# Kernel tuning notes

Hardware: AMD Instinct MI355X
Metric: run time of the kernel (lower is better)

The kernel has to match this reference:

```python
import jax, jax.numpy as jnp
import numpy as np

N = 65536      # nodes in batched graph
E = 2097152    # edges (avg degree 32)
V = 1000       # chord vocabulary size
F_IN = 128     # chord feature dim
H = 256        # hidden_dim
OUT = 128      # out_dim
G = 256        # number of graphs in batch


def _gcn_layer(x, W, b, row, col, norm, n):
    # x: [n, f_in] -> [n, f_out]; PyG GCNConv: linear then normalized aggregation + bias
    x = x @ W
    msg = x[row] * norm[:, None]            # gather at source, scale by sym-norm
    return jax.ops.segment_sum(msg, col, num_segments=n) + b


def setup_inputs() -> dict:
    key = jax.random.key(0)
    ks = jax.random.split(key, 9)
    chord_feats = jax.random.normal(ks[0], (V, F_IN), jnp.float32)
    W1 = jax.random.normal(ks[1], (F_IN, H), jnp.float32) * 0.05
    b1 = jnp.zeros((H,), jnp.float32)
    W2 = jax.random.normal(ks[2], (H, OUT), jnp.float32) * 0.05
    b2 = jnp.zeros((OUT,), jnp.float32)
    edge_attr = jax.random.uniform(ks[3], (E,), jnp.float32)          # positive edge weights
    node_indices = jax.random.randint(ks[4], (N,), 0, V, jnp.int64)
    edge_index = jax.random.randint(ks[5], (2, E), 0, N, jnp.int64)
    batch_index = jnp.sort(jax.random.randint(ks[6], (N,), 0, G, jnp.int64))
    return {"chord_feats": chord_feats, "W1": W1, "b1": b1, "W2": W2, "b2": b2,
            "edge_attr": edge_attr, "node_indices": node_indices,
            "edge_index": edge_index, "batch_index": batch_index}


def reference(chord_feats, W1, b1, W2, b2, edge_attr, node_indices, edge_index, batch_index):
    loops = jnp.arange(N, dtype=edge_index.dtype)
    row = jnp.concatenate([edge_index[0], loops])   # source
    col = jnp.concatenate([edge_index[1], loops])   # target
    ew = jnp.concatenate([edge_attr, jnp.ones((N,), edge_attr.dtype)])  # self-loop weight 1
    # symmetric GCN normalization: D^-1/2 A D^-1/2
    deg = jax.ops.segment_sum(ew, col, num_segments=N)
    dis = jnp.where(deg > 0, jax.lax.rsqrt(jnp.maximum(deg, 1e-30)), 0.0)
    norm = dis[row] * ew * dis[col]

    x = chord_feats[node_indices]                   # [N, F_IN]
    x = jax.nn.relu(_gcn_layer(x, W1, b1, row, col, norm, N))
    x = jax.nn.relu(_gcn_layer(x, W2, b2, row, col, norm, N))

    # global_mean_pool over batch_index
    sums = jax.ops.segment_sum(x, batch_index, num_segments=G)
    counts = jax.ops.segment_sum(jnp.ones((N,), x.dtype), batch_index, num_segments=G)
    return sums / jnp.maximum(counts, 1.0)[:, None]
```

## Files before the change

kernel.cpp:

```cpp
#include <hip/hip_runtime.h>
#include <hip/hip_fp16.h>
#include <math.h>

constexpr int N_NODES = 65536;
constexpr int N_EDGES = 2097152;
constexpr int F_IN    = 128;
constexpr int H_DIM   = 256;
constexpr int O_DIM   = 128;
constexpr int N_GRAPH = 256;
constexpr int V_SIZE  = 1000;

constexpr int EPB  = 8192;
constexpr int NBLK = N_EDGES / EPB;
constexpr float FXP = 16777216.0f;

typedef _Float16 half8 __attribute__((ext_vector_type(8)));
typedef float floatx4 __attribute__((ext_vector_type(4)));


__global__ void k_init(float* __restrict__ pool, const int* __restrict__ batch,
                       float* __restrict__ cntf, const float* __restrict__ cf,
                       const float* __restrict__ W1, __half* __restrict__ cfW1,
                       const float* __restrict__ W2, _Float16* __restrict__ W2T) {
    __shared__ float xs[8 * F_IN];
    int i = blockIdx.x * blockDim.x + threadIdx.x;
    if (i < N_GRAPH * O_DIM) pool[i] = 0.0f;
    if (blockIdx.x == 0) {
        int g = threadIdx.x;
        int lo = 0, hi = N_NODES;
        while (lo < hi) { int m = (lo + hi) >> 1; if (batch[m] < g) lo = m + 1; else hi = m; }
        int start = lo;
        lo = 0; hi = N_NODES;
        while (lo < hi) { int m = (lo + hi) >> 1; if (batch[m] <= g) lo = m + 1; else hi = m; }
        cntf[g] = (float)(lo - start);
    }
    if (blockIdx.x < V_SIZE / 8) {
        int rb = blockIdx.x * 8;
        int t  = threadIdx.x;
        #pragma unroll
        for (int p = 0; p < 4; ++p) {
            int idx = p * 256 + t;
            int r = idx >> 7, k = idx & 127;
            xs[idx] = cf[(size_t)(rb + r) * F_IN + k];
        }
        __syncthreads();
        float acc[8] = {};
        for (int k = 0; k < F_IN; ++k) {
            float w = W1[k * H_DIM + t];
            #pragma unroll
            for (int j = 0; j < 8; ++j) acc[j] += xs[j * F_IN + k] * w;
        }
        #pragma unroll
        for (int j = 0; j < 8; ++j)
            cfW1[(size_t)(rb + j) * H_DIM + t] = __float2half(acc[j]);
    }
    if (blockIdx.x >= 128) {
        int idx = (blockIdx.x - 128) * 256 + threadIdx.x;
        int nn = idx >> 8, kk = idx & 255;
        W2T[idx] = (_Float16)W2[kk * O_DIM + nn];
    }
}


__global__ void k_hist(const int* __restrict__ col, int* __restrict__ hist) {
    __shared__ int h[256];
    int t = threadIdx.x;
    h[t] = 0;
    __syncthreads();
    int base = blockIdx.x * EPB;
    #pragma unroll
    for (int i = 0; i < EPB / 256; ++i)
        atomicAdd(&h[col[base + i * 256 + t] >> 8], 1);
    __syncthreads();
    hist[t * NBLK + blockIdx.x] = h[t];
}


__global__ void k_scan1(const int* __restrict__ in, int* __restrict__ out,
                        int* __restrict__ bsum) {
    __shared__ int s[256];
    int tid = threadIdx.x;
    int i = blockIdx.x * 256 + tid;
    int v = in[i];
    s[tid] = v;
    __syncthreads();
    for (int d = 1; d < 256; d <<= 1) {
        int t = (tid >= d) ? s[tid - d] : 0;
        __syncthreads();
        s[tid] += t;
        __syncthreads();
    }
    out[i] = s[tid] - v;
    if (tid == 255) bsum[blockIdx.x] = s[255];
}

__global__ void k_scan2(int* __restrict__ bsum) {
    __shared__ int s[256];
    int tid = threadIdx.x;
    int v = bsum[tid];
    s[tid] = v;
    __syncthreads();
    for (int d = 1; d < 256; d <<= 1) {
        int t = (tid >= d) ? s[tid - d] : 0;
        __syncthreads();
        s[tid] += t;
        __syncthreads();
    }
    bsum[tid] = s[tid] - v;
}


__global__ void k_part(const int* __restrict__ row, const int* __restrict__ col,
                       const float* __restrict__ ew, const int* __restrict__ nidx,
                       const int* __restrict__ hoffs, const int* __restrict__ bsum,
                       int2* __restrict__ part) {
    __shared__ int cur[256];
    int t = threadIdx.x;
    cur[t] = hoffs[t * NBLK + blockIdx.x] + bsum[t];
    __syncthreads();
    int base = blockIdx.x * EPB;
    for (int i = 0; i < EPB / 256; ++i) {
        int e = base + i * 256 + t;
        int r = row[e], c = col[e];
        unsigned hw = (unsigned)__half_as_ushort(__float2half(ew[e]));
        int vb = nidx[r];
        int slot = atomicAdd(&cur[c >> 8], 1);
        int2 rec;
        rec.x = (r << 16) | ((c & 255) << 8) | (vb >> 2);
        rec.y = (int)(((unsigned)(vb & 3) << 16) | hw);
        part[slot] = rec;
    }
}


__global__ void k_build1(const int* __restrict__ hoffs, const int* __restrict__ bsum,
                         const int2* __restrict__ part, float* __restrict__ dis,
                         int* __restrict__ offs) {
    __shared__ unsigned long long dc[256];
    __shared__ int sc[256];
    int t = threadIdx.x;
    int bucket = blockIdx.x;
    dc[t] = 0ULL;
    __syncthreads();
    int start = hoffs[bucket * NBLK] + bsum[bucket];
    int end   = (bucket == 255) ? N_EDGES : (hoffs[(bucket + 1) * NBLK] + bsum[bucket + 1]);
    for (int j = start + t; j < end; j += 256) {
        int2 rec = part[j];
        int dst = (rec.x >> 8) & 255;
        float w = __half2float(__ushort_as_half((unsigned short)(rec.y & 0xFFFF)));
        atomicAdd(&dc[dst], (1ULL << 40) |
                  (unsigned long long)(unsigned)(w * FXP + 0.5f));
    }
    __syncthreads();
    unsigned long long v = dc[t];
    float deg = 1.0f + (float)(v & 0xFFFFFFFFFFULL) * (1.0f / FXP);
    dis[bucket * 256 + t] = 1.0f / sqrtf(deg);
    int cnt = (int)(v >> 40);
    sc[t] = cnt;
    __syncthreads();
    for (int d = 1; d < 256; d <<= 1) {
        int x = (t >= d) ? sc[t - d] : 0;
        __syncthreads();
        sc[t] += x;
        __syncthreads();
    }
    offs[bucket * 256 + t] = start + sc[t] - cnt;
    if (bucket == 255 && t == 255) offs[N_NODES] = N_EDGES;
}


__global__ void k_build2(const int* __restrict__ hoffs, const int* __restrict__ bsum,
                         const int2* __restrict__ part, const float* __restrict__ dis,
                         const int* __restrict__ offs, int2* __restrict__ csr) {
    __shared__ int cur[256];
    int t = threadIdx.x;
    int bucket = blockIdx.x;
    cur[t] = offs[bucket * 256 + t];
    __syncthreads();
    int start = hoffs[bucket * NBLK] + bsum[bucket];
    int end   = (bucket == 255) ? N_EDGES : (hoffs[(bucket + 1) * NBLK] + bsum[bucket + 1]);
    for (int j = start + t; j < end; j += 256) {
        int2 rec = part[j];
        int dst = (rec.x >> 8) & 255;
        unsigned src = ((unsigned)rec.x) >> 16;
        int vb = ((rec.x & 255) << 2) | ((rec.y >> 16) & 3);
        float w = __half2float(__ushort_as_half((unsigned short)(rec.y & 0xFFFF)));
        float nm = dis[src] * w;
        int slot = atomicAdd(&cur[dst], 1);
        int2 e;
        e.x = (int)((src << 10) | (unsigned)vb);
        e.y = __float_as_int(nm);
        csr[slot] = e;
    }
}

__device__ __forceinline__ void acc8(float* e, int4 v, float n) {
    float2 f0 = __half22float2(*(__half2*)&v.x);
    float2 f1 = __half22float2(*(__half2*)&v.y);
    float2 f2 = __half22float2(*(__half2*)&v.z);
    float2 f3 = __half22float2(*(__half2*)&v.w);
    e[0] += f0.x * n; e[1] += f0.y * n;
    e[2] += f1.x * n; e[3] += f1.y * n;
    e[4] += f2.x * n; e[5] += f2.y * n;
    e[6] += f3.x * n; e[7] += f3.y * n;
}


__global__ void __launch_bounds__(256) k_agg1g2(
        const int4* __restrict__ cfW1, const int* __restrict__ nidx,
        const float* __restrict__ dis, const int* __restrict__ offs,
        const int2* __restrict__ csr, const float4* __restrict__ b1f4,
        const _Float16* __restrict__ W2T, __half* __restrict__ xw2h) {
    __shared__ _Float16 h1s[16 * 264];
    int wave = threadIdx.x >> 6;
    int lane = threadIdx.x & 63;
    int g    = lane >> 5;
    int sl   = lane & 31;
    int rowbase = blockIdx.x * 16;

    float4 bb0 = b1f4[2 * sl];
    float4 bb1 = b1f4[2 * sl + 1];

    for (int j = 0; j < 4; ++j) {
        int c = rowbase + wave * 4 + j;
        float d = dis[c];
        int4 sp = cfW1[(size_t)nidx[c] * 32 + sl];
        float esum[8] = {0.f, 0.f, 0.f, 0.f, 0.f, 0.f, 0.f, 0.f};
        int a0 = offs[c], a1 = offs[c + 1];
        int s = a0;
        if (s < a1 && (s & 1)) {
            int sb = __builtin_amdgcn_readfirstlane(s);
            int2 e0 = csr[sb];
            int4 v0 = cfW1[(size_t)(e0.x & 1023) * 32 + sl];
            float n = (g == 0) ? __int_as_float(e0.y) : 0.0f;
            acc8(esum, v0, n);
            ++s;
        }
        for (; s + 8 <= a1; s += 8) {
            int sb = __builtin_amdgcn_readfirstlane(s);
            int4 ee[4];
            #pragma unroll
            for (int u = 0; u < 4; ++u) ee[u] = *(const int4*)(csr + sb + 2 * u);
            int4 v[4]; float n[4];
            #pragma unroll
            for (int u = 0; u < 4; ++u) {
                int ex = g ? ee[u].z : ee[u].x;
                int ey = g ? ee[u].w : ee[u].y;
                n[u] = __int_as_float(ey);
                v[u] = cfW1[(size_t)(ex & 1023) * 32 + sl];
            }
            #pragma unroll
            for (int u = 0; u < 4; ++u) acc8(esum, v[u], n[u]);
        }
        for (; s + 2 <= a1; s += 2) {
            int sb = __builtin_amdgcn_readfirstlane(s);
            int4 ee = *(const int4*)(csr + sb);
            int ex = g ? ee.z : ee.x;
            int ey = g ? ee.w : ee.y;
            int4 v0 = cfW1[(size_t)(ex & 1023) * 32 + sl];
            acc8(esum, v0, __int_as_float(ey));
        }
        if (s < a1) {
            int sb = __builtin_amdgcn_readfirstlane(s);
            int2 e0 = csr[sb];
            int4 v0 = cfW1[(size_t)(e0.x & 1023) * 32 + sl];
            float n = (g == 0) ? __int_as_float(e0.y) : 0.0f;
            acc8(esum, v0, n);
        }
        #pragma unroll
        for (int k = 0; k < 8; ++k) esum[k] += __shfl_xor(esum[k], 32, 64);

        float dd = d * d;
        float2 s0 = __half22float2(*(__half2*)&sp.x);
        float2 s1 = __half22float2(*(__half2*)&sp.y);
        float2 s2 = __half22float2(*(__half2*)&sp.z);
        float2 s3 = __half22float2(*(__half2*)&sp.w);
        float r[8];
        r[0] = bb0.x + s0.x * dd + d * esum[0];
        r[1] = bb0.y + s0.y * dd + d * esum[1];
        r[2] = bb0.z + s1.x * dd + d * esum[2];
        r[3] = bb0.w + s1.y * dd + d * esum[3];
        r[4] = bb1.x + s2.x * dd + d * esum[4];
        r[5] = bb1.y + s2.y * dd + d * esum[5];
        r[6] = bb1.z + s3.x * dd + d * esum[6];
        r[7] = bb1.w + s3.y * dd + d * esum[7];
        #pragma unroll
        for (int k = 0; k < 8; ++k) r[k] = r[k] > 0.f ? r[k] : 0.f;
        float2 p0 = {r[0], r[1]}, p1 = {r[2], r[3]}, p2 = {r[4], r[5]}, p3 = {r[6], r[7]};
        __half2 h0 = __float22half2_rn(p0);
        __half2 h1v = __float22half2_rn(p1);
        __half2 h2 = __float22half2_rn(p2);
        __half2 h3 = __float22half2_rn(p3);
        int4 outv;
        outv.x = *(int*)&h0;
        outv.y = *(int*)&h1v;
        outv.z = *(int*)&h2;
        outv.w = *(int*)&h3;
        if (lane < 32)
            *(int4*)&h1s[(wave * 4 + j) * 264 + sl * 8] = outv;
    }
    __syncthreads();

    int quad = lane >> 4;
    int n    = lane & 15;
    half8 a[8];
    #pragma unroll
    for (int kt = 0; kt < 8; ++kt)
        a[kt] = *(const half8*)&h1s[n * 264 + kt * 32 + quad * 8];
    #pragma unroll
    for (int t2 = 0; t2 < 2; ++t2) {
        int nt = wave * 2 + t2;
        floatx4 acc = {0.f, 0.f, 0.f, 0.f};
        const _Float16* brow = W2T + (size_t)(nt * 16 + n) * H_DIM;
        #pragma unroll
        for (int kt = 0; kt < 8; ++kt) {
            half8 b = *(const half8*)(brow + kt * 32 + quad * 8);
            acc = __builtin_amdgcn_mfma_f32_16x16x32_f16(a[kt], b, acc, 0, 0, 0);
        }
        #pragma unroll
        for (int r = 0; r < 4; ++r) {
            int rowi = rowbase + quad * 4 + r;
            xw2h[(size_t)rowi * O_DIM + nt * 16 + n] = __float2half(acc[r]);
        }
    }
}


__global__ void k_agg2_pool(const int4* __restrict__ xw2h, const float* __restrict__ b2,
                            const float* __restrict__ dis, const int* __restrict__ offs,
                            const int2* __restrict__ csr, const int* __restrict__ batch,
                            float* __restrict__ pool) {
    __shared__ float red[4][128];
    __shared__ int bgs[4];
    int wave = threadIdx.x >> 6;
    int lane = threadIdx.x & 63;
    int grp  = lane >> 4;
    int sl   = lane & 15;
    int c = blockIdx.x * 4 + wave;
    float d = dis[c];
    int4 sp = xw2h[(size_t)c * 16 + sl];
    float esum[8] = {0.f, 0.f, 0.f, 0.f, 0.f, 0.f, 0.f, 0.f};
    int s0 = offs[c], s1 = offs[c + 1];
    int s = s0;
    for (; s + 32 <= s1; s += 32) {
        int sb = __builtin_amdgcn_readfirstlane(s);
        int2 e[8];
        #pragma unroll
        for (int u = 0; u < 8; ++u) {
            long long rr = __builtin_nontemporal_load((const long long*)(csr + sb + 4 * u + grp));
            e[u] = *(int2*)&rr;
        }
        int4 v[8];
        #pragma unroll
        for (int u = 0; u < 8; ++u)
            v[u] = xw2h[(size_t)(((unsigned)e[u].x) >> 10) * 16 + sl];
        #pragma unroll
        for (int u = 0; u < 8; ++u) acc8(esum, v[u], __int_as_float(e[u].y));
    }
    for (; s + 4 <= s1; s += 4) {
        int sb = __builtin_amdgcn_readfirstlane(s);
        int2 e0 = csr[sb + grp];
        int4 v0 = xw2h[(size_t)(((unsigned)e0.x) >> 10) * 16 + sl];
        acc8(esum, v0, __int_as_float(e0.y));
    }
    if (s < s1) {
        int sb = __builtin_amdgcn_readfirstlane(s);
        int idx = sb + grp;
        int idc = idx < s1 ? idx : s1 - 1;
        int2 e0 = csr[idc];
        int4 v0 = xw2h[(size_t)(((unsigned)e0.x) >> 10) * 16 + sl];
        float n = (idx < s1) ? __int_as_float(e0.y) : 0.0f;
        acc8(esum, v0, n);
    }
    #pragma unroll
    for (int k = 0; k < 8; ++k) {
        esum[k] += __shfl_xor(esum[k], 16, 64);
        esum[k] += __shfl_xor(esum[k], 32, 64);
    }
    float dd = d * d;
    float2 f0 = __half22float2(*(__half2*)&sp.x);
    float2 f1 = __half22float2(*(__half2*)&sp.y);
    float2 f2 = __half22float2(*(__half2*)&sp.z);
    float2 f3 = __half22float2(*(__half2*)&sp.w);
    float4 bb0 = ((const float4*)b2)[2 * sl];
    float4 bb1 = ((const float4*)b2)[2 * sl + 1];
    float acc[8];
    acc[0] = bb0.x + f0.x * dd + d * esum[0];
    acc[1] = bb0.y + f0.y * dd + d * esum[1];
    acc[2] = bb0.z + f1.x * dd + d * esum[2];
    acc[3] = bb0.w + f1.y * dd + d * esum[3];
    acc[4] = bb1.x + f2.x * dd + d * esum[4];
    acc[5] = bb1.y + f2.y * dd + d * esum[5];
    acc[6] = bb1.z + f3.x * dd + d * esum[6];
    acc[7] = bb1.w + f3.y * dd + d * esum[7];
    #pragma unroll
    for (int k = 0; k < 8; ++k) acc[k] = acc[k] > 0.f ? acc[k] : 0.f;
    if (grp == 0) {
        #pragma unroll
        for (int k = 0; k < 8; ++k) red[wave][8 * sl + k] = acc[k];
    }
    if (lane == 0) bgs[wave] = batch[c];
    __syncthreads();
    if (wave == 0) {
        float2 a;
        a.x = red[0][2 * lane];
        a.y = red[0][2 * lane + 1];
        int cg = bgs[0];
        #pragma unroll
        for (int w = 1; w < 4; ++w) {
            int g = bgs[w];
            float2 r;
            r.x = red[w][2 * lane];
            r.y = red[w][2 * lane + 1];
            if (g == cg) { a.x += r.x; a.y += r.y; }
            else {
                atomicAdd(&pool[cg * O_DIM + 2 * lane], a.x);
                atomicAdd(&pool[cg * O_DIM + 2 * lane + 1], a.y);
                a = r; cg = g;
            }
        }
        atomicAdd(&pool[cg * O_DIM + 2 * lane], a.x);
        atomicAdd(&pool[cg * O_DIM + 2 * lane + 1], a.y);
    }
}

__global__ void k_final(const float* __restrict__ pool, const float* __restrict__ cnt,
                        float* __restrict__ out) {
    int t = blockIdx.x * blockDim.x + threadIdx.x;
    if (t < N_GRAPH * O_DIM) {
        int g = t / O_DIM;
        out[t] = pool[t] / fmaxf(cnt[g], 1.0f);
    }
}


extern "C" void kernel_launch(void* const* d_in, const int* in_sizes, int n_in,
                              void* d_out, int out_size, void* d_ws, size_t ws_size,
                              hipStream_t stream) {
    const float* cf   = (const float*)d_in[0];
    const float* W1   = (const float*)d_in[1];
    const float* b1   = (const float*)d_in[2];
    const float* W2   = (const float*)d_in[3];
    const float* b2   = (const float*)d_in[4];
    const float* ew   = (const float*)d_in[5];
    const int*   nidx = (const int*)d_in[6];
    const int*   eidx = (const int*)d_in[7];
    const int*   bidx = (const int*)d_in[8];
    float* out = (float*)d_out;

    const int* row = eidx;
    const int* col = eidx + N_EDGES;

    char* ws = (char*)d_ws;
    size_t off = 0;
    int*   hist  = (int*)  (ws + off); off += (size_t)N_NODES * 4;
    int*   hoffs = (int*)  (ws + off); off += (size_t)N_NODES * 4;
    int*   bsum  = (int*)  (ws + off); off += 4096;
    float* dis   = (float*)(ws + off); off += (size_t)N_NODES * 4;
    int*   offs  = (int*)  (ws + off); off += (size_t)(N_NODES + 16) * 4;
    int2*  csr   = (int2*) (ws + off); off += (size_t)N_EDGES * 8;
    float* pool  = (float*)(ws + off); off += (size_t)(N_GRAPH * O_DIM + N_GRAPH) * 4;
    __half* cfW1 = (__half*)(ws + off); off += (size_t)V_SIZE * H_DIM * 2;
    _Float16* W2T = (_Float16*)(ws + off); off += (size_t)O_DIM * H_DIM * 2;
    off = (off + 255) & ~(size_t)255;
    int2*  part  = (int2*) (ws + off); off += (size_t)N_EDGES * 8;
    __half* xw2h = (__half*)part;
    float* cntf  = pool + N_GRAPH * O_DIM;

    k_init<<<256, 256, 0, stream>>>(pool, bidx, cntf, cf, W1, cfW1, W2, W2T);
    k_hist<<<NBLK, 256, 0, stream>>>(col, hist);
    k_scan1<<<256, 256, 0, stream>>>(hist, hoffs, bsum);
    k_scan2<<<1, 256, 0, stream>>>(bsum);

    k_part<<<NBLK, 256, 0, stream>>>(row, col, ew, nidx, hoffs, bsum, part);
    k_build1<<<256, 256, 0, stream>>>(hoffs, bsum, part, dis, offs);
    k_build2<<<256, 256, 0, stream>>>(hoffs, bsum, part, dis, offs, csr);

    k_agg1g2<<<N_NODES / 16, 256, 0, stream>>>((const int4*)cfW1, nidx, dis, offs, csr,
                                               (const float4*)b1, W2T, xw2h);

    k_agg2_pool<<<N_NODES / 4, 256, 0, stream>>>((const int4*)xw2h, b2, dis, offs, csr,
                                                 bidx, pool);

    k_final<<<(N_GRAPH * O_DIM + 255) / 256, 256, 0, stream>>>(pool, cntf, out);
}
```

Measured before the change: 374.1 us.

## Compute degrees with global atomics in histogram and split CSR build across more blocks

Degree accumulation moves out of the bucket-local build1 pass and into the histogram kernel, using global 64-bit atomics per target node, so one full pass over the partitioned edges disappears. Edges per block drop so the histogram and partition kernels launch four times as many blocks, and the second-level scan now handles four entries per thread. The CSR scatter kernel splits each bucket across four blocks that share global cursors, which trades shared-memory atomics for global ones. The layer-2 aggregation loop unroll is halved and its nontemporal edge loads become ordinary loads.

Result: slower. 439.2 us (+17.4%).

```diff
diff --git a/kernel.cpp b/kernel.cpp
--- a/kernel.cpp
+++ b/kernel.cpp
@@ -10,7 +10,7 @@
 constexpr int N_GRAPH = 256;
 constexpr int V_SIZE  = 1000;
 
-constexpr int EPB  = 8192;
+constexpr int EPB  = 2048;
 constexpr int NBLK = N_EDGES / EPB;
 constexpr float FXP = 16777216.0f;
 
@@ -21,10 +21,12 @@
 __global__ void k_init(float* __restrict__ pool, const int* __restrict__ batch,
                        float* __restrict__ cntf, const float* __restrict__ cf,
                        const float* __restrict__ W1, __half* __restrict__ cfW1,
-                       const float* __restrict__ W2, _Float16* __restrict__ W2T) {
+                       const float* __restrict__ W2, _Float16* __restrict__ W2T,
+                       unsigned long long* __restrict__ dc) {
     __shared__ float xs[8 * F_IN];
     int i = blockIdx.x * blockDim.x + threadIdx.x;
     if (i < N_GRAPH * O_DIM) pool[i] = 0.0f;
+    dc[i] = 0ULL;
     if (blockIdx.x == 0) {
         int g = threadIdx.x;
         int lo = 0, hi = N_NODES;
@@ -62,15 +64,22 @@
 }
 
 
-__global__ void k_hist(const int* __restrict__ col, int* __restrict__ hist) {
+__global__ void k_hist(const int* __restrict__ col, const float* __restrict__ ew,
+                       int* __restrict__ hist, unsigned long long* __restrict__ dc) {
     __shared__ int h[256];
     int t = threadIdx.x;
     h[t] = 0;
     __syncthreads();
     int base = blockIdx.x * EPB;
     #pragma unroll
-    for (int i = 0; i < EPB / 256; ++i)
-        atomicAdd(&h[col[base + i * 256 + t] >> 8], 1);
+    for (int i = 0; i < EPB / 256; ++i) {
+        int e = base + i * 256 + t;
+        int c = col[e];
+        atomicAdd(&h[c >> 8], 1);
+        float w = __half2float(__float2half(ew[e]));
+        atomicAdd(&dc[c], (1ULL << 40) |
+                  (unsigned long long)(unsigned)(w * FXP + 0.5f));
+    }
     __syncthreads();
     hist[t * NBLK + blockIdx.x] = h[t];
 }
@@ -96,17 +105,22 @@
 
 __global__ void k_scan2(int* __restrict__ bsum) {
     __shared__ int s[256];
-    int tid = threadIdx.x;
-    int v = bsum[tid];
-    s[tid] = v;
+    int t = threadIdx.x;
+    int4 v = *(int4*)&bsum[4 * t];
+    int tsum = v.x + v.y + v.z + v.w;
+    s[t] = tsum;
     __syncthreads();
     for (int d = 1; d < 256; d <<= 1) {
-        int t = (tid >= d) ? s[tid - d] : 0;
-        __syncthreads();
-        s[tid] += t;
-        __syncthreads();
-    }
-    bsum[tid] = s[tid] - v;
+        int x = (t >= d) ? s[t - d] : 0;
+        __syncthreads();
+        s[t] += x;
+        __syncthreads();
+    }
+    int ex = s[t] - tsum;
+    bsum[4 * t]     = ex;
+    bsum[4 * t + 1] = ex + v.x;
+    bsum[4 * t + 2] = ex + v.x + v.y;
+    bsum[4 * t + 3] = ex + v.x + v.y + v.z;
 }
 
 
@@ -116,7 +130,8 @@
                        int2* __restrict__ part) {
     __shared__ int cur[256];
     int t = threadIdx.x;
-    cur[t] = hoffs[t * NBLK + blockIdx.x] + bsum[t];
+    int idx = t * NBLK + blockIdx.x;
+    cur[t] = hoffs[idx] + bsum[idx >> 8];
     __syncthreads();
     int base = blockIdx.x * EPB;
     for (int i = 0; i < EPB / 256; ++i) {
@@ -133,28 +148,17 @@
 }
 
 
-__global__ void k_build1(const int* __restrict__ hoffs, const int* __restrict__ bsum,
-                         const int2* __restrict__ part, float* __restrict__ dis,
-                         int* __restrict__ offs) {
-    __shared__ unsigned long long dc[256];
+__global__ void k_disoffs(const unsigned long long* __restrict__ dc,
+                          const int* __restrict__ hoffs, const int* __restrict__ bsum,
+                          float* __restrict__ dis, int* __restrict__ offs,
+                          int* __restrict__ gcur) {
     __shared__ int sc[256];
     int t = threadIdx.x;
     int bucket = blockIdx.x;
-    dc[t] = 0ULL;
-    __syncthreads();
-    int start = hoffs[bucket * NBLK] + bsum[bucket];
-    int end   = (bucket == 255) ? N_EDGES : (hoffs[(bucket + 1) * NBLK] + bsum[bucket + 1]);
-    for (int j = start + t; j < end; j += 256) {
-        int2 rec = part[j];
-        int dst = (rec.x >> 8) & 255;
-        float w = __half2float(__ushort_as_half((unsigned short)(rec.y & 0xFFFF)));
-        atomicAdd(&dc[dst], (1ULL << 40) |
-                  (unsigned long long)(unsigned)(w * FXP + 0.5f));
-    }
-    __syncthreads();
-    unsigned long long v = dc[t];
+    unsigned long long v = dc[bucket * 256 + t];
     float deg = 1.0f + (float)(v & 0xFFFFFFFFFFULL) * (1.0f / FXP);
     dis[bucket * 256 + t] = 1.0f / sqrtf(deg);
+    int bstart = hoffs[bucket * NBLK] + bsum[bucket * 4];
     int cnt = (int)(v >> 40);
     sc[t] = cnt;
     __syncthreads();
@@ -164,29 +168,32 @@
         sc[t] += x;
         __syncthreads();
     }
-    offs[bucket * 256 + t] = start + sc[t] - cnt;
+    int o = bstart + sc[t] - cnt;
+    offs[bucket * 256 + t] = o;
+    gcur[bucket * 256 + t] = o;
     if (bucket == 255 && t == 255) offs[N_NODES] = N_EDGES;
 }
 
 
-__global__ void k_build2(const int* __restrict__ hoffs, const int* __restrict__ bsum,
-                         const int2* __restrict__ part, const float* __restrict__ dis,
-                         const int* __restrict__ offs, int2* __restrict__ csr) {
-    __shared__ int cur[256];
+__global__ void k_build2g(const int* __restrict__ hoffs, const int* __restrict__ bsum,
+                          const int2* __restrict__ part, const float* __restrict__ dis,
+                          int* __restrict__ gcur, int2* __restrict__ csr) {
     int t = threadIdx.x;
-    int bucket = blockIdx.x;
-    cur[t] = offs[bucket * 256 + t];
-    __syncthreads();
-    int start = hoffs[bucket * NBLK] + bsum[bucket];
-    int end   = (bucket == 255) ? N_EDGES : (hoffs[(bucket + 1) * NBLK] + bsum[bucket + 1]);
-    for (int j = start + t; j < end; j += 256) {
+    int bucket = blockIdx.x >> 2, q = blockIdx.x & 3;
+    int bstart = hoffs[bucket * NBLK] + bsum[bucket * 4];
+    int bend   = (bucket == 255) ? N_EDGES
+                                 : hoffs[(bucket + 1) * NBLK] + bsum[(bucket + 1) * 4];
+    int len = bend - bstart;
+    int qs = bstart + ((len * q) >> 2);
+    int qe = bstart + ((len * (q + 1)) >> 2);
+    for (int j = qs + t; j < qe; j += 256) {
         int2 rec = part[j];
         int dst = (rec.x >> 8) & 255;
         unsigned src = ((unsigned)rec.x) >> 16;
         int vb = ((rec.x & 255) << 2) | ((rec.y >> 16) & 3);
         float w = __half2float(__ushort_as_half((unsigned short)(rec.y & 0xFFFF)));
         float nm = dis[src] * w;
-        int slot = atomicAdd(&cur[dst], 1);
+        int slot = atomicAdd(&gcur[(bucket << 8) | dst], 1);
         int2 e;
         e.x = (int)((src << 10) | (unsigned)vb);
         e.y = __float_as_int(nm);
@@ -342,20 +349,17 @@
     float esum[8] = {0.f, 0.f, 0.f, 0.f, 0.f, 0.f, 0.f, 0.f};
     int s0 = offs[c], s1 = offs[c + 1];
     int s = s0;
-    for (; s + 32 <= s1; s += 32) {
+    for (; s + 16 <= s1; s += 16) {
         int sb = __builtin_amdgcn_readfirstlane(s);
-        int2 e[8];
-        #pragma unroll
-        for (int u = 0; u < 8; ++u) {
-            long long rr = __builtin_nontemporal_load((const long long*)(csr + sb + 4 * u + grp));
-            e[u] = *(int2*)&rr;
-        }
-        int4 v[8];
-        #pragma unroll
-        for (int u = 0; u < 8; ++u)
+        int2 e[4];
+        #pragma unroll
+        for (int u = 0; u < 4; ++u) e[u] = csr[sb + 4 * u + grp];
+        int4 v[4];
+        #pragma unroll
+        for (int u = 0; u < 4; ++u)
             v[u] = xw2h[(size_t)(((unsigned)e[u].x) >> 10) * 16 + sl];
         #pragma unroll
-        for (int u = 0; u < 8; ++u) acc8(esum, v[u], __int_as_float(e[u].y));
+        for (int u = 0; u < 4; ++u) acc8(esum, v[u], __int_as_float(e[u].y));
     }
     for (; s + 4 <= s1; s += 4) {
         int sb = __builtin_amdgcn_readfirstlane(s);
@@ -453,11 +457,14 @@
 
     char* ws = (char*)d_ws;
     size_t off = 0;
-    int*   hist  = (int*)  (ws + off); off += (size_t)N_NODES * 4;
-    int*   hoffs = (int*)  (ws + off); off += (size_t)N_NODES * 4;
-    int*   bsum  = (int*)  (ws + off); off += 4096;
+    int*   hist  = (int*)  (ws + off); off += (size_t)256 * NBLK * 4;
+    int*   hoffs = (int*)  (ws + off); off += (size_t)256 * NBLK * 4;
+    int*   bsum  = (int*)  (ws + off); off += (size_t)NBLK * 4;
+    unsigned long long* dc = (unsigned long long*)(ws + off);
+    off += (size_t)N_NODES * 8;
     float* dis   = (float*)(ws + off); off += (size_t)N_NODES * 4;
     int*   offs  = (int*)  (ws + off); off += (size_t)(N_NODES + 16) * 4;
+    int*   gcur  = (int*)  (ws + off); off += (size_t)N_NODES * 4;
     int2*  csr   = (int2*) (ws + off); off += (size_t)N_EDGES * 8;
     float* pool  = (float*)(ws + off); off += (size_t)(N_GRAPH * O_DIM + N_GRAPH) * 4;
     __half* cfW1 = (__half*)(ws + off); off += (size_t)V_SIZE * H_DIM * 2;
@@ -467,14 +474,14 @@
     __half* xw2h = (__half*)part;
     float* cntf  = pool + N_GRAPH * O_DIM;
 
-    k_init<<<256, 256, 0, stream>>>(pool, bidx, cntf, cf, W1, cfW1, W2, W2T);
-    k_hist<<<NBLK, 256, 0, stream>>>(col, hist);
-    k_scan1<<<256, 256, 0, stream>>>(hist, hoffs, bsum);
+    k_init<<<256, 256, 0, stream>>>(pool, bidx, cntf, cf, W1, cfW1, W2, W2T, dc);
+    k_hist<<<NBLK, 256, 0, stream>>>(col, ew, hist, dc);
+    k_scan1<<<256 * NBLK / 256, 256, 0, stream>>>(hist, hoffs, bsum);
     k_scan2<<<1, 256, 0, stream>>>(bsum);
 
+    k_disoffs<<<256, 256, 0, stream>>>(dc, hoffs, bsum, dis, offs, gcur);
     k_part<<<NBLK, 256, 0, stream>>>(row, col, ew, nidx, hoffs, bsum, part);
-    k_build1<<<256, 256, 0, stream>>>(hoffs, bsum, part, dis, offs);
-    k_build2<<<256, 256, 0, stream>>>(hoffs, bsum, part, dis, offs, csr);
+    k_build2g<<<1024, 256, 0, stream>>>(hoffs, bsum, part, dis, gcur, csr);
 
     k_agg1g2<<<N_NODES / 16, 256, 0, stream>>>((const int4*)cfW1, nidx, dis, offs, csr,
                                                (const float4*)b1, W2T, xw2h);
```
